# Kernel optimization log

Measured on AMD Instinct MI355X. Metric: run time of the kernel, lower is better.

## Reference

```python
import jax, jax.numpy as jnp
import numpy as np
from jax import lax

BN_EPS = 1e-5
TERN_FRAC = 0.7  # TBN threshold: delta = 0.7 * mean(|x|)

def batchnorm(x, gamma, beta, mean, var):
    # eval-mode BN over channel dim (NCHW)
    inv = gamma * lax.rsqrt(var + BN_EPS)
    return x * inv[None, :, None, None] + (beta - mean * inv)[None, :, None, None]

def ternarize(x):
    # STE: forward = ternary {-1,0,+1} with threshold 0.7*mean|x|; backward = identity
    delta = TERN_FRAC * jnp.mean(jnp.abs(x))
    q = jnp.where(x > delta, 1.0, jnp.where(x < -delta, -1.0, 0.0)).astype(x.dtype)
    return x + lax.stop_gradient(q - x)

def binarize_weight(w):
    # per-output-channel scale alpha = mean|w|, w_b = alpha * sign(w); STE backward
    alpha = jnp.mean(jnp.abs(w), axis=(1, 2, 3), keepdims=True)
    q = alpha * jnp.sign(w)
    return w + lax.stop_gradient(q - w)

def tbn_conv(x, w, stride):
    xq = ternarize(x)
    wq = binarize_weight(w)
    return lax.conv_general_dilated(
        xq, wq, window_strides=(stride, stride), padding=((1, 1), (1, 1)),
        dimension_numbers=("NCHW", "OIHW", "NCHW"))

def setup_inputs() -> dict:
    key = jax.random.key(0)
    ks = jax.random.split(key, 6)
    B, C, H, W = 32, 256, 32, 32
    x = jax.random.normal(ks[0], (B, C, H, W), dtype=jnp.float32)
    w1 = jax.random.normal(ks[1], (C, C, 3, 3), dtype=jnp.float32) * 0.05
    w2 = jax.random.normal(ks[2], (C, C, 3, 3), dtype=jnp.float32) * 0.05
    return {
        "x": x, "w1": w1, "w2": w2,
        "gamma1": jnp.ones((C,), jnp.float32), "beta1": jnp.zeros((C,), jnp.float32),
        "mean1": jax.random.normal(ks[3], (C,), jnp.float32) * 0.1,
        "var1": jax.random.uniform(ks[4], (C,), jnp.float32) + 0.5,
        "gamma2": jnp.ones((C,), jnp.float32), "beta2": jnp.zeros((C,), jnp.float32),
        "mean2": jax.random.normal(ks[5], (C,), jnp.float32) * 0.1,
        "var2": jax.random.uniform(jax.random.fold_in(key, 7), (C,), jnp.float32) + 0.5,
    }

def reference(x, w1, w2, gamma1, beta1, mean1, var1, gamma2, beta2, mean2, var2):
    # x = ShortCut(x, conv1(relu1(bn1(x))))  [relu = Identity]
    h = x + tbn_conv(batchnorm(x, gamma1, beta1, mean1, var1), w1, 1)
    # x = x + conv2(relu2(bn2(x)))
    out = h + tbn_conv(batchnorm(h, gamma2, beta2, mean2, var2), w2, 1)
    return out
```

## Files before the change

kernel.cpp:

```cpp
#include <hip/hip_runtime.h>

#define BN_EPS 1e-5f
#define SR_STEP  16384
#define BQ_KC    8704
#define KSCALE   (0.7f / 8388608.0f)

typedef __attribute__((ext_vector_type(4))) int int32x4;

__global__ void frontend_kernel(const float* __restrict__ w1,
                                signed char* __restrict__ Sr1,
                                float* __restrict__ alpha1,
                                const float* __restrict__ w2,
                                signed char* __restrict__ Sr2,
                                float* __restrict__ alpha2,
                                const float* __restrict__ x,
                                const float* __restrict__ gamma,
                                const float* __restrict__ beta,
                                const float* __restrict__ mean,
                                const float* __restrict__ var,
                                float* __restrict__ partials) {
    __shared__ __align__(16) signed char lsg[9][256];
    __shared__ float red[256];
    int bid = blockIdx.x;
    int tid = threadIdx.x;

    if (bid < 512) {
        int set = bid >> 8;
        const float* w = set ? w2 : w1;
        signed char* Sr = set ? Sr2 : Sr1;
        float* alpha = set ? alpha2 : alpha1;
        int o = bid & 255;
        const float* wp = w + (o * 256 + tid) * 9;
        float s = 0.f;
#pragma unroll
        for (int j = 0; j < 9; ++j) {
            float v = wp[j];
            s += fabsf(v);
            lsg[j][tid] = v > 0.f ? 1 : (v < 0.f ? -1 : 0);
        }
        red[tid] = s;
        __syncthreads();
        for (int off = 128; off > 0; off >>= 1) {
            if (tid < off) red[tid] += red[tid + off];
            __syncthreads();
        }
        if (tid == 0) alpha[o] = red[0] / 2304.0f;
        if (tid < 144) {
            int t = tid / 16, u = tid % 16;
            int c0 = u * 16;
            int kc = c0 >> 6, cb = c0 & 63;
            int32x4 v = *(const int32x4*)(&lsg[t][c0]);
            *(int32x4*)(Sr + (size_t)((t * 4 + kc) * 256 + o) * 64 + cb) = v;
        }
    } else {
        int rid = bid - 512;
        const float4* x4 = (const float4*)x;
        float s = 0.f;
        int base = rid * 256 + tid;
#pragma unroll
        for (int k = 0; k < 4; ++k) {
            int i = base + k * 524288;
            int c = (i >> 8) & 255;
            float inv = gamma[c] * rsqrtf(var[c] + BN_EPS);
            float b = beta[c] - mean[c] * inv;
            float4 v = x4[i];
            s += fabsf(v.x * inv + b) + fabsf(v.y * inv + b) +
                 fabsf(v.z * inv + b) + fabsf(v.w * inv + b);
        }
        red[tid] = s;
        __syncthreads();
        for (int off = 128; off > 0; off >>= 1) {
            if (tid < off) red[tid] += red[tid + off];
            __syncthreads();
        }
        if (tid == 0) partials[rid] = red[0];
    }
}

template <bool FUSE>
__global__ __launch_bounds__(256, 3) void tbn_conv_kernel(
    const float* __restrict__ src,
    const signed char* __restrict__ Sr,
    const float* __restrict__ alpha,
    float* __restrict__ out,
    const float* __restrict__ dpart, int nPart,
    const float* __restrict__ qg, const float* __restrict__ qb,
    const float* __restrict__ qm, const float* __restrict__ qv,
    const float* __restrict__ fg, const float* __restrict__ fbt,
    const float* __restrict__ fm, const float* __restrict__ fv,
    float* __restrict__ partials) {
    __shared__ __align__(16) char smem[39936];
    signed char* Bq = (signed char*)smem;
    float* red  = (float*)smem;
    float* sInv = (float*)(smem + 34816);
    float* sB   = (float*)(smem + 35840);
    float* sAl  = (float*)(smem + 36864);
    float* sInvS= (float*)(smem + 37888);
    float* sBS  = (float*)(smem + 38912);

    int bid = blockIdx.x;
    int wg = (bid & 7) * 64 + (bid >> 3);
    int n = wg >> 4;
    int pb = wg & 15;
    int tid = threadIdx.x, lane = tid & 63, wid = tid >> 6;
    int l15 = lane & 15, kg = lane >> 4;
    int y0 = pb * 2;

    {
        float inv = qg[tid] * rsqrtf(qv[tid] + BN_EPS);
        sInv[tid] = inv;
        sB[tid] = qb[tid] - qm[tid] * inv;
        sAl[tid] = alpha[tid];
        if (FUSE) {
            float finv = fg[tid] * rsqrtf(fv[tid] + BN_EPS);
            sInvS[tid] = finv;
            sBS[tid] = fbt[tid] - fm[tid] * finv;
        }
    }
    float s = 0.f;
    for (int i = tid; i < nPart; i += 256) s += dpart[i];
    red[tid] = s;
    __syncthreads();
    for (int off = 128; off > 0; off >>= 1) {
        if (tid < off) red[tid] += red[tid + off];
        __syncthreads();
    }
    float delta = red[0] * KSCALE;
    __syncthreads();

    const float4* src4 = (const float4*)src + (size_t)n * 65536;
#pragma unroll
    for (int k = 0; k < 2; ++k) {
        int idx = tid + 256 * k;
        int quad = idx & 7;
        int cg = (idx >> 3) & 15;
        int row = idx >> 7;
        int absrow = y0 + row - 1;
        int wrd[4][4];
#pragma unroll
        for (int px = 0; px < 4; ++px)
#pragma unroll
            for (int d = 0; d < 4; ++d) wrd[px][d] = 0;
        if (absrow >= 0 && absrow < 32) {
#pragma unroll
            for (int j = 0; j < 16; ++j) {
                int c = cg * 16 + j;
                float4 v = src4[(size_t)c * 256 + absrow * 8 + quad];
                float inv = sInv[c], bb = sB[c];
                float va[4] = {v.x, v.y, v.z, v.w};
#pragma unroll
                for (int px = 0; px < 4; ++px) {
                    float t = va[px] * inv + bb;
                    int q = t > delta ? 1 : (t < -delta ? -1 : 0);
                    wrd[px][j >> 2] |= (q & 255) << (8 * (j & 3));
                }
            }
        }
        int kc = cg >> 2, kgp = cg & 3;
#pragma unroll
        for (int px = 0; px < 4; ++px) {
            int slot = quad * 4 + px + 1;
            int dst = kc * BQ_KC + row * 2176 + slot * 64 +
                      (((kgp + (slot >> 1)) & 3) << 4);
            int32x4 vv;
            vv[0] = wrd[px][0]; vv[1] = wrd[px][1];
            vv[2] = wrd[px][2]; vv[3] = wrd[px][3];
            *(int32x4*)(&Bq[dst]) = vv;
        }
    }
    if (tid < 128) {
        int cg = tid & 15;
        int rest = tid >> 4;
        int row = rest >> 1, side = rest & 1;
        int slot = side ? 33 : 0;
        int kc = cg >> 2, kgp = cg & 3;
        int dst = kc * BQ_KC + row * 2176 + slot * 64 +
                  (((kgp + (slot >> 1)) & 3) << 4);
        int32x4 z; z[0] = 0; z[1] = 0; z[2] = 0; z[3] = 0;
        *(int32x4*)(&Bq[dst]) = z;
    }
    __syncthreads();

    int o0 = wid * 64;
    const signed char* Abase = Sr + (size_t)(o0 + l15) * 64 + kg * 16;

    int32x4 acc[4][4];
#pragma unroll
    for (int m = 0; m < 4; ++m)
#pragma unroll
        for (int nn = 0; nn < 4; ++nn) {
            acc[m][nn][0] = 0; acc[m][nn][1] = 0;
            acc[m][nn][2] = 0; acc[m][nn][3] = 0;
        }

    int32x4 fa[3][4], fb[2][4];

#define GLD(D, P) \
    asm volatile("global_load_dwordx4 %0, %1, off" : "=v"(D) : "v"(P))
#define SLAB(I) ((((I) % 9) * 4) + ((I) / 9))
#define LOADA(I)                                                              \
    do {                                                                      \
        const signed char* pa_ = Abase + (size_t)SLAB(I) * SR_STEP;           \
        GLD(fa[(I) % 3][0], pa_);                                             \
        GLD(fa[(I) % 3][1], pa_ + 1024);                                      \
        GLD(fa[(I) % 3][2], pa_ + 2048);                                      \
        GLD(fa[(I) % 3][3], pa_ + 3072);                                      \
    } while (0)
#define LOADB(J, BUF)                                                         \
    do {                                                                      \
        const int kcj_ = (J) / 9, tj_ = (J) % 9;                              \
        const int kh_ = tj_ / 3 - 1, kw_ = tj_ % 3 - 1;                       \
        _Pragma("unroll")                                                     \
        for (int nn = 0; nn < 4; ++nn) {                                      \
            const int row_ = (nn >> 1) + 1 + kh_;                             \
            int slot_ = (nn & 1) * 16 + l15 + 1 + kw_;                        \
            int off_ = kcj_ * BQ_KC + row_ * 2176 + slot_ * 64 +              \
                       (((kg + (slot_ >> 1)) & 3) << 4);                      \
            fb[BUF][nn] = *(const int32x4*)(&Bq[off_]);                       \
        }                                                                     \
    } while (0)
#define MFMA16(I, BUF)                                                        \
    do {                                                                      \
        _Pragma("unroll")                                                     \
        for (int m = 0; m < 4; ++m)                                           \
            _Pragma("unroll")                                                 \
            for (int nn = 0; nn < 4; ++nn)                                    \
                acc[m][nn] = __builtin_amdgcn_mfma_i32_16x16x64_i8(           \
                    fa[(I) % 3][m], fb[BUF][nn], acc[m][nn], 0, 0, 0);        \
    } while (0)
#define WAITV(N)                                                              \
    do { asm volatile("s_waitcnt vmcnt(" #N ")" ::: "memory");                \
         __builtin_amdgcn_sched_barrier(0); } while (0)

    LOADA(0); LOADA(1); LOADA(2);
    LOADB(0, 0);
#pragma unroll
    for (int i = 0; i < 36; ++i) {
        if (i <= 33)      WAITV(8);
        else if (i == 34) WAITV(4);
        else              WAITV(0);
        if (i < 35) LOADB(i + 1, (i + 1) & 1);
        MFMA16(i, i & 1);
        if (i + 3 <= 35) LOADA(i + 3);
    }
#undef GLD
#undef SLAB
#undef LOADA
#undef LOADB
#undef MFMA16
#undef WAITV

    float psum = 0.f;
#pragma unroll
    for (int m = 0; m < 4; ++m) {
#pragma unroll
        for (int r = 0; r < 4; ++r) {
            int o = wid * 64 + m * 16 + kg * 4 + r;
            float al = sAl[o];
            float inv = 0.f, bb = 0.f;
            if (FUSE) { inv = sInvS[o]; bb = sBS[o]; }
            const float* rp = src + (size_t)n * 262144 + (size_t)o * 1024;
            float* op = out + (size_t)n * 262144 + (size_t)o * 1024;
#pragma unroll
            for (int nn = 0; nn < 4; ++nn) {
                int p = pb * 64 + nn * 16 + l15;
                float hv = rp[p] + al * (float)acc[m][nn][r];
                op[p] = hv;
                if (FUSE) psum += fabsf(hv * inv + bb);
            }
        }
    }
    if (FUSE) {
        __syncthreads();
        red[tid] = psum;
        __syncthreads();
        for (int off = 128; off > 0; off >>= 1) {
            if (tid < off) red[tid] += red[tid + off];
            __syncthreads();
        }
        if (tid == 0) partials[wg] = red[0];
    }
}

extern "C" void kernel_launch(void* const* d_in, const int* in_sizes, int n_in,
                              void* d_out, int out_size, void* d_ws, size_t ws_size,
                              hipStream_t stream) {
    (void)in_sizes; (void)n_in; (void)out_size; (void)ws_size;
    const float* x  = (const float*)d_in[0];
    const float* w1 = (const float*)d_in[1];
    const float* w2 = (const float*)d_in[2];
    const float* g1 = (const float*)d_in[3];
    const float* b1 = (const float*)d_in[4];
    const float* m1 = (const float*)d_in[5];
    const float* v1 = (const float*)d_in[6];
    const float* g2 = (const float*)d_in[7];
    const float* b2 = (const float*)d_in[8];
    const float* m2 = (const float*)d_in[9];
    const float* v2 = (const float*)d_in[10];
    float* out = (float*)d_out;
    char* ws = (char*)d_ws;

    float* red1   = (float*)(ws + 4096);
    float* redc   = (float*)(ws + 16384);
    float* alpha1 = (float*)(ws + 28672);
    float* alpha2 = (float*)(ws + 29696);
    signed char* Sr1 = (signed char*)(ws + ((size_t)1 << 20));
    signed char* Sr2 = (signed char*)(ws + ((size_t)2 << 20));
    float* h         = (float*)(ws + ((size_t)4 << 20));

    frontend_kernel<<<2560, 256, 0, stream>>>(w1, Sr1, alpha1, w2, Sr2, alpha2,
                                              x, g1, b1, m1, v1, red1);
    tbn_conv_kernel<true><<<512, 256, 0, stream>>>(
        x, Sr1, alpha1, h, red1, 2048,
        g1, b1, m1, v1, g2, b2, m2, v2, redc);
    tbn_conv_kernel<false><<<512, 256, 0, stream>>>(
        h, Sr2, alpha2, out, redc, 512,
        g2, b2, m2, v2, g2, b2, m2, v2, redc);
}
```

Before: 79.96 us.

## Retile TBN conv block to 128 output channels by 4 rows

```diff
diff --git a/kernel.cpp b/kernel.cpp
--- a/kernel.cpp
+++ b/kernel.cpp
@@ -2,7 +2,7 @@
 
 #define BN_EPS 1e-5f
 #define SR_STEP  16384
-#define BQ_KC    8704
+#define BQ_KC    13056
 #define KSCALE   (0.7f / 8388608.0f)
 
 typedef __attribute__((ext_vector_type(4))) int int32x4;
@@ -78,7 +78,7 @@
 }
 
 template <bool FUSE>
-__global__ __launch_bounds__(256, 3) void tbn_conv_kernel(
+__global__ __launch_bounds__(256, 2) void tbn_conv_kernel(
     const float* __restrict__ src,
     const signed char* __restrict__ Sr,
     const float* __restrict__ alpha,
@@ -89,32 +89,36 @@
     const float* __restrict__ fg, const float* __restrict__ fbt,
     const float* __restrict__ fm, const float* __restrict__ fv,
     float* __restrict__ partials) {
-    __shared__ __align__(16) char smem[39936];
+    __shared__ __align__(16) char smem[55808];
     signed char* Bq = (signed char*)smem;
     float* red  = (float*)smem;
-    float* sInv = (float*)(smem + 34816);
-    float* sB   = (float*)(smem + 35840);
-    float* sAl  = (float*)(smem + 36864);
-    float* sInvS= (float*)(smem + 37888);
-    float* sBS  = (float*)(smem + 38912);
+    float* sInv = (float*)(smem + 52224);
+    float* sB   = (float*)(smem + 53248);
+    float* sAl  = (float*)(smem + 54272);
+    float* sInvS= (float*)(smem + 54784);
+    float* sBS  = (float*)(smem + 55296);
 
     int bid = blockIdx.x;
     int wg = (bid & 7) * 64 + (bid >> 3);
     int n = wg >> 4;
-    int pb = wg & 15;
+    int ob = (wg >> 3) & 1;
+    int pb = wg & 7;
     int tid = threadIdx.x, lane = tid & 63, wid = tid >> 6;
     int l15 = lane & 15, kg = lane >> 4;
-    int y0 = pb * 2;
+    int y0 = pb * 4;
 
     {
         float inv = qg[tid] * rsqrtf(qv[tid] + BN_EPS);
         sInv[tid] = inv;
         sB[tid] = qb[tid] - qm[tid] * inv;
-        sAl[tid] = alpha[tid];
+    }
+    if (tid < 128) {
+        int o = ob * 128 + tid;
+        sAl[tid] = alpha[o];
         if (FUSE) {
-            float finv = fg[tid] * rsqrtf(fv[tid] + BN_EPS);
+            float finv = fg[o] * rsqrtf(fv[o] + BN_EPS);
             sInvS[tid] = finv;
-            sBS[tid] = fbt[tid] - fm[tid] * finv;
+            sBS[tid] = fbt[o] - fm[o] * finv;
         }
     }
     float s = 0.f;
@@ -130,10 +134,10 @@
 
     const float4* src4 = (const float4*)src + (size_t)n * 65536;
 #pragma unroll
-    for (int k = 0; k < 2; ++k) {
+    for (int k = 0; k < 3; ++k) {
         int idx = tid + 256 * k;
         int quad = idx & 7;
-        int cg = (idx >> 3) & 15;
+        int cg2 = (idx >> 3) & 15;
         int row = idx >> 7;
         int absrow = y0 + row - 1;
         int wrd[4][4];
@@ -144,7 +148,7 @@
         if (absrow >= 0 && absrow < 32) {
 #pragma unroll
             for (int j = 0; j < 16; ++j) {
-                int c = cg * 16 + j;
+                int c = cg2 * 16 + j;
                 float4 v = src4[(size_t)c * 256 + absrow * 8 + quad];
                 float inv = sInv[c], bb = sB[c];
                 float va[4] = {v.x, v.y, v.z, v.w};
@@ -156,7 +160,7 @@
                 }
             }
         }
-        int kc = cg >> 2, kgp = cg & 3;
+        int kc = cg2 >> 2, kgp = cg2 & 3;
 #pragma unroll
         for (int px = 0; px < 4; ++px) {
             int slot = quad * 4 + px + 1;
@@ -168,12 +172,12 @@
             *(int32x4*)(&Bq[dst]) = vv;
         }
     }
-    if (tid < 128) {
-        int cg = tid & 15;
+    if (tid < 192) {
+        int cg2 = tid & 15;
         int rest = tid >> 4;
         int row = rest >> 1, side = rest & 1;
         int slot = side ? 33 : 0;
-        int kc = cg >> 2, kgp = cg & 3;
+        int kc = cg2 >> 2, kgp = cg2 & 3;
         int dst = kc * BQ_KC + row * 2176 + slot * 64 +
                   (((kgp + (slot >> 1)) & 3) << 4);
         int32x4 z; z[0] = 0; z[1] = 0; z[2] = 0; z[3] = 0;
@@ -181,19 +185,19 @@
     }
     __syncthreads();
 
-    int o0 = wid * 64;
+    int o0 = ob * 128 + wid * 32;
     const signed char* Abase = Sr + (size_t)(o0 + l15) * 64 + kg * 16;
 
-    int32x4 acc[4][4];
-#pragma unroll
-    for (int m = 0; m < 4; ++m)
-#pragma unroll
-        for (int nn = 0; nn < 4; ++nn) {
+    int32x4 acc[2][8];
+#pragma unroll
+    for (int m = 0; m < 2; ++m)
+#pragma unroll
+        for (int nn = 0; nn < 8; ++nn) {
             acc[m][nn][0] = 0; acc[m][nn][1] = 0;
             acc[m][nn][2] = 0; acc[m][nn][3] = 0;
         }
 
-    int32x4 fa[3][4], fb[2][4];
+    int32x4 fa[3][2], fb[2][8];
 
 #define GLD(D, P) \
     asm volatile("global_load_dwordx4 %0, %1, off" : "=v"(D) : "v"(P))
@@ -203,15 +207,13 @@
         const signed char* pa_ = Abase + (size_t)SLAB(I) * SR_STEP;           \
         GLD(fa[(I) % 3][0], pa_);                                             \
         GLD(fa[(I) % 3][1], pa_ + 1024);                                      \
-        GLD(fa[(I) % 3][2], pa_ + 2048);                                      \
-        GLD(fa[(I) % 3][3], pa_ + 3072);                                      \
     } while (0)
 #define LOADB(J, BUF)                                                         \
     do {                                                                      \
         const int kcj_ = (J) / 9, tj_ = (J) % 9;                              \
         const int kh_ = tj_ / 3 - 1, kw_ = tj_ % 3 - 1;                       \
         _Pragma("unroll")                                                     \
-        for (int nn = 0; nn < 4; ++nn) {                                      \
+        for (int nn = 0; nn < 8; ++nn) {                                      \
             const int row_ = (nn >> 1) + 1 + kh_;                             \
             int slot_ = (nn & 1) * 16 + l15 + 1 + kw_;                        \
             int off_ = kcj_ * BQ_KC + row_ * 2176 + slot_ * 64 +              \
@@ -222,9 +224,9 @@
 #define MFMA16(I, BUF)                                                        \
     do {                                                                      \
         _Pragma("unroll")                                                     \
-        for (int m = 0; m < 4; ++m)                                           \
+        for (int m = 0; m < 2; ++m)                                           \
             _Pragma("unroll")                                                 \
-            for (int nn = 0; nn < 4; ++nn)                                    \
+            for (int nn = 0; nn < 8; ++nn)                                    \
                 acc[m][nn] = __builtin_amdgcn_mfma_i32_16x16x64_i8(           \
                     fa[(I) % 3][m], fb[BUF][nn], acc[m][nn], 0, 0, 0);        \
     } while (0)
@@ -236,8 +238,8 @@
     LOADB(0, 0);
 #pragma unroll
     for (int i = 0; i < 36; ++i) {
-        if (i <= 33)      WAITV(8);
-        else if (i == 34) WAITV(4);
+        if (i <= 33)      WAITV(4);
+        else if (i == 34) WAITV(2);
         else              WAITV(0);
         if (i < 35) LOADB(i + 1, (i + 1) & 1);
         MFMA16(i, i & 1);
@@ -252,18 +254,19 @@
 
     float psum = 0.f;
 #pragma unroll
-    for (int m = 0; m < 4; ++m) {
+    for (int m = 0; m < 2; ++m) {
 #pragma unroll
         for (int r = 0; r < 4; ++r) {
-            int o = wid * 64 + m * 16 + kg * 4 + r;
-            float al = sAl[o];
+            int oLoc = wid * 32 + m * 16 + kg * 4 + r;
+            int o = ob * 128 + oLoc;
+            float al = sAl[oLoc];
             float inv = 0.f, bb = 0.f;
-            if (FUSE) { inv = sInvS[o]; bb = sBS[o]; }
+            if (FUSE) { inv = sInvS[oLoc]; bb = sBS[oLoc]; }
             const float* rp = src + (size_t)n * 262144 + (size_t)o * 1024;
             float* op = out + (size_t)n * 262144 + (size_t)o * 1024;
 #pragma unroll
-            for (int nn = 0; nn < 4; ++nn) {
-                int p = pb * 64 + nn * 16 + l15;
+            for (int nn = 0; nn < 8; ++nn) {
+                int p = pb * 128 + nn * 16 + l15;
                 float hv = rp[p] + al * (float)acc[m][nn][r];
                 op[p] = hv;
                 if (FUSE) psum += fabsf(hv * inv + bb);
```

Result: faster. 69.67 us (-12.9%).
